# Kernel tuning notes

Measured on AMD Instinct MI355X. Metric: run time of the kernel, lower is better.

## Reference

```python
import jax, jax.numpy as jnp
import numpy as np

D_MODEL = 1024
N_HEADS = 16
HEAD_DIM = D_MODEL // N_HEADS
D_FF = 4096
MAX_STEPS = 16
MAX_LEN = 64  # hardcoded in the module
LN_EPS = 1e-5


def _layer_norm(x, g, b):
    m = jnp.mean(x, axis=-1, keepdims=True)
    v = jnp.mean((x - m) ** 2, axis=-1, keepdims=True)
    return (x - m) * jax.lax.rsqrt(v + LN_EPS) * g + b


def setup_inputs() -> dict:
    key = jax.random.key(0)
    ks = jax.random.split(key, 12)
    B, S = 8, 1024
    std = 0.02
    return {
        "x": jax.random.normal(ks[0], (B, S, D_MODEL), dtype=jnp.float32),
        "step_embed": jax.random.normal(ks[1], (MAX_STEPS, D_MODEL), dtype=jnp.float32) * std,
        "qkv_w": jax.random.normal(ks[2], (D_MODEL, 3 * D_MODEL), dtype=jnp.float32) * std,
        "qkv_b": jnp.zeros((3 * D_MODEL,), dtype=jnp.float32),
        "out_w": jax.random.normal(ks[3], (D_MODEL, D_MODEL), dtype=jnp.float32) * std,
        "out_b": jnp.zeros((D_MODEL,), dtype=jnp.float32),
        "rel_pos_bias": jax.random.normal(ks[4], (2 * MAX_LEN - 1,), dtype=jnp.float32) * std,
        "w1": jax.random.normal(ks[5], (D_MODEL, D_FF), dtype=jnp.float32) * std,
        "b1": jnp.zeros((D_FF,), dtype=jnp.float32),
        "w2": jax.random.normal(ks[6], (D_FF, D_MODEL), dtype=jnp.float32) * std,
        "b2": jnp.zeros((D_MODEL,), dtype=jnp.float32),
        "ln1_g": jnp.ones((D_MODEL,), dtype=jnp.float32),
        "ln1_b": jnp.zeros((D_MODEL,), dtype=jnp.float32),
        "ln2_g": jnp.ones((D_MODEL,), dtype=jnp.float32),
        "ln2_b": jnp.zeros((D_MODEL,), dtype=jnp.float32),
        "think_step": 3,
    }


def reference(x, step_embed, qkv_w, qkv_b, out_w, out_b, rel_pos_bias,
              w1, b1, w2, b2, ln1_g, ln1_b, ln2_g, ln2_b, think_step):
    B, S, D = x.shape
    scale = HEAD_DIM ** -0.5

    # step embedding (clamped), broadcast over batch and sequence
    step = min(int(think_step), MAX_STEPS - 1)
    x = x + step_embed[step][None, None, :]

    # QKV projection -> (3, B, H, S, Dh)
    qkv = (x @ qkv_w + qkv_b).reshape(B, S, 3, N_HEADS, HEAD_DIM)
    qkv = jnp.transpose(qkv, (2, 0, 3, 1, 4))
    q, k, v = qkv[0], qkv[1], qkv[2]

    # attention scores with clamped relative-position bias
    scores = jnp.einsum("bhqd,bhkd->bhqk", q, k) * scale
    pos = jnp.arange(S)
    rel = jnp.clip(pos[:, None] - pos[None, :] + (MAX_LEN - 1), 0, 2 * MAX_LEN - 2)
    scores = scores + rel_pos_bias[rel][None, None, :, :]

    probs = jax.nn.softmax(scores, axis=-1)
    attn = jnp.einsum("bhqk,bhkd->bhqd", probs, v)
    attn = jnp.transpose(attn, (0, 2, 1, 3)).reshape(B, S, D)
    attn = attn @ out_w + out_b

    x = _layer_norm(x + attn, ln1_g, ln1_b)
    ffn = jax.nn.gelu(x @ w1 + b1, approximate=False) @ w2 + b2
    x = _layer_norm(x + ffn, ln2_g, ln2_b)
    return x
```

## Files before the change

### kernel.cpp

```cpp
#include <hip/hip_runtime.h>
#include <cstdint>
#include <cmath>

typedef unsigned short u16;
typedef unsigned int u32;
typedef __bf16 bf16x8 __attribute__((ext_vector_type(8)));
typedef float f32x4 __attribute__((ext_vector_type(4)));
typedef float f32x16 __attribute__((ext_vector_type(16)));

#define DEV __device__ __forceinline__

DEV u16 f2bf(float f) {
    union { float f; unsigned u; } a; a.f = f;
    unsigned u = a.u;
    return (u16)((u + 0x7FFFu + ((u >> 16) & 1u)) >> 16);
}

DEV u32 pack2bf(float a, float b) {
    union { float f; u32 u; } ua, ub; ua.f = a; ub.f = b;
    return __builtin_amdgcn_perm(ub.u + 0x8000u, ua.u + 0x8000u, 0x07060302u);
}

DEV float fast_exp2(float x) {
    float r;
    asm("v_exp_f32 %0, %1" : "=v"(r) : "v"(x));
    return r;
}

DEV void async16(void* lds, const void* g) {
    __builtin_amdgcn_global_load_lds(
        (const __attribute__((address_space(1))) unsigned int*)g,
        (__attribute__((address_space(3))) unsigned int*)lds, 16, 0, 0);
}

#define LOG2E 1.44269504088896f

__global__ __launch_bounds__(256)
void prep_k(const float* __restrict__ s0, u16* __restrict__ d0,
            const float* __restrict__ s1, u16* __restrict__ d1,
            const float* __restrict__ s2, u16* __restrict__ d2,
            const float* __restrict__ s3, u16* __restrict__ d3,
            const float* __restrict__ x, const float* __restrict__ se,
            const int* __restrict__ ts, float* __restrict__ xo, u16* __restrict__ xb) {
    int b = blockIdx.x, tid = threadIdx.x;
    if (b < 12288) {
        __shared__ float tile[32][33];
        const float* src; u16* dst; int N, tidx;
        if (b < 3072)      { src = s0; dst = d0; N = 3072; tidx = b; }
        else if (b < 4096) { src = s1; dst = d1; N = 1024; tidx = b - 3072; }
        else if (b < 8192) { src = s2; dst = d2; N = 4096; tidx = b - 4096; }
        else               { src = s3; dst = d3; N = 1024; tidx = b - 8192; }
        int ntx = N >> 5;
        int n0 = (tidx % ntx) * 32, k0 = (tidx / ntx) * 32;
        int K = (b >= 8192) ? 4096 : 1024;
        int tx = tid & 31, ty = tid >> 5;
        #pragma unroll
        for (int i = ty; i < 32; i += 8) tile[i][tx] = src[(size_t)(k0 + i) * N + n0 + tx];
        __syncthreads();
        #pragma unroll
        for (int i = ty; i < 32; i += 8) dst[(size_t)(n0 + i) * K + k0 + tx] = f2bf(tile[tx][i]);
    } else {
        int st = ts[0]; st = st < 0 ? 0 : (st > 15 ? 15 : st);
        size_t i = (size_t)(b - 12288) * 256 + tid;
        float4 v = ((const float4*)x)[i];
        int c = (int)(i & 255);
        float4 e = ((const float4*)(se + (size_t)st * 1024))[c];
        v.x += e.x; v.y += e.y; v.z += e.z; v.w += e.w;
        ((float4*)xo)[i] = v;
        ushort4 u; u.x = f2bf(v.x); u.y = f2bf(v.y); u.z = f2bf(v.z); u.w = f2bf(v.w);
        ((ushort4*)xb)[i] = u;
    }
}

template<int EPI>
__global__ __launch_bounds__(256)
void gemm_bt(const u16* __restrict__ A, const u16* __restrict__ Bt,
             const float* __restrict__ bias, int Kdim,
             u16* __restrict__ ob0, u16* __restrict__ ob1, u16* __restrict__ ob2,
             const float* __restrict__ addf, float* __restrict__ outf) {
    __shared__ __align__(16) u16 lA[128 * 64];
    __shared__ __align__(16) u16 lB[128 * 64];
    const int tid = threadIdx.x, wave = tid >> 6, lane = tid & 63;
    const int m5 = lane & 31, h = lane >> 5;
    const int wm = wave >> 1, wn = wave & 1;
    const size_t m0 = (size_t)blockIdx.x * 128, n0 = (size_t)blockIdx.y * 128;
    const size_t kb = (size_t)Kdim * 2;

    f32x16 acc[2][2];
    #pragma unroll
    for (int i = 0; i < 2; i++)
        #pragma unroll
        for (int j = 0; j < 2; j++)
            #pragma unroll
            for (int e = 0; e < 16; e++) acc[i][j][e] = 0.f;

    const char* Ab = (const char*)A + m0 * kb;
    const char* Bb = (const char*)Bt + n0 * kb;

    auto stage = [&](const char* srcbase, u16* ldsb, int k0) {
        #pragma unroll
        for (int j = 0; j < 4; j++) {
            int loff = wave * 4096 + j * 1024 + lane * 16;
            int L = loff >> 4, r = L >> 3, c = L & 7, g = c ^ (r & 7);
            async16((char*)ldsb + loff, srcbase + (size_t)r * kb + (size_t)k0 * 2 + g * 16);
        }
    };

    stage(Ab, lA, 0); stage(Bb, lB, 0);
    const int r7 = m5 & 7;
    for (int k0 = 0; k0 < Kdim; k0 += 64) {
        __syncthreads();
        bf16x8 af[2][4], bfr[2][4];
        #pragma unroll
        for (int ti = 0; ti < 2; ti++) {
            int rowA = wm * 64 + ti * 32 + m5;
            int rowB = wn * 64 + ti * 32 + m5;
            #pragma unroll
            for (int kh = 0; kh < 4; kh++) {
                int cs = (kh * 2 + h) ^ r7;
                af[ti][kh]  = *(const bf16x8*)((const char*)lA + rowA * 128 + cs * 16);
                bfr[ti][kh] = *(const bf16x8*)((const char*)lB + rowB * 128 + cs * 16);
            }
        }
        __syncthreads();
        if (k0 + 64 < Kdim) { stage(Ab, lA, k0 + 64); stage(Bb, lB, k0 + 64); }
        #pragma unroll
        for (int kh = 0; kh < 4; kh++)
            #pragma unroll
            for (int ti = 0; ti < 2; ti++)
                #pragma unroll
                for (int tj = 0; tj < 2; tj++)
                    acc[ti][tj] = __builtin_amdgcn_mfma_f32_32x32x16_bf16(
                        af[ti][kh], bfr[tj][kh], acc[ti][tj], 0, 0, 0);
    }

    #pragma unroll
    for (int ti = 0; ti < 2; ti++) {
        #pragma unroll
        for (int tj = 0; tj < 2; tj++) {
            size_t col = n0 + wn * 64 + tj * 32 + m5;
            float bv = bias[col];
            if constexpr (EPI == 0) {
                size_t t = col >> 10, c = col & 1023, hh = c >> 6, dh = c & 63;
                #pragma unroll
                for (int g = 0; g < 4; g++) {
                    size_t row0 = m0 + wm * 64 + ti * 32 + 4 * h + 8 * g;
                    size_t bq = row0 >> 10, s0 = row0 & 1023;
                    if (t == 0) {
                        #pragma unroll
                        for (int r = 0; r < 4; r++)
                            ob0[((bq * 16 + hh) * 1024 + s0 + r) * 64 + dh] =
                                f2bf((acc[ti][tj][g * 4 + r] + bv) * 0.18033688011112f);
                    } else if (t == 1) {
                        #pragma unroll
                        for (int r = 0; r < 4; r++)
                            ob1[((bq * 16 + hh) * 1024 + s0 + r) * 64 + dh] =
                                f2bf(acc[ti][tj][g * 4 + r] + bv);
                    } else {
                        ushort4 tmp;
                        tmp.x = f2bf(acc[ti][tj][g * 4 + 0] + bv);
                        tmp.y = f2bf(acc[ti][tj][g * 4 + 1] + bv);
                        tmp.z = f2bf(acc[ti][tj][g * 4 + 2] + bv);
                        tmp.w = f2bf(acc[ti][tj][g * 4 + 3] + bv);
                        *(ushort4*)(ob2 + ((bq * 16 + hh) * 64 + dh) * 1024 + s0) = tmp;
                    }
                }
            } else {
                #pragma unroll
                for (int g = 0; g < 4; g++) {
                    #pragma unroll
                    for (int r = 0; r < 4; r++) {
                        size_t row = m0 + wm * 64 + ti * 32 + 4 * h + 8 * g + r;
                        float val = acc[ti][tj][g * 4 + r] + bv;
                        if constexpr (EPI == 1) {
                            size_t o = row * 1024 + col;
                            outf[o] = addf[o] + val;
                        } else if constexpr (EPI == 2) {
                            float ge = 0.5f * val * (1.f + erff(val * 0.70710678118f));
                            ob0[row * 4096 + col] = f2bf(ge);
                        } else {
                            size_t o = row * 1024 + col;
                            outf[o] = addf[o] + val;
                        }
                    }
                }
            }
        }
    }
}

__global__ __launch_bounds__(256, 2)
void attn_k(const u16* __restrict__ Q, const u16* __restrict__ K_, const u16* __restrict__ Vt,
            const float* __restrict__ relb, u16* __restrict__ Out) {
    __shared__ __align__(16) u16 sP[128 * 128];
    __shared__ __align__(16) u16 sK[128 * 64];
    __shared__ __align__(16) u16 sVt[64 * 128];
    __shared__ float sL[4][128];
    __shared__ float sLinv[128];
    __shared__ float sRel[128];

    const int tid = threadIdx.x, wave = tid >> 6, lane = tid & 63;
    const int m5 = lane & 31, h = lane >> 5;
    const int bh = blockIdx.x, q0 = blockIdx.y * 128;
    const size_t base = (size_t)bh * 65536;

    if (tid < 127) sRel[tid] = relb[tid] * LOG2E;

    auto stageK = [&](int kv0) {
        const char* kbp = (const char*)(K_ + base + (size_t)kv0 * 64);
        #pragma unroll
        for (int j = 0; j < 4; j++) {
            int loff = wave * 4096 + j * 1024 + lane * 16;
            int L = loff >> 4, r = L >> 3, c = L & 7, g = c ^ (r & 7);
            async16((char*)sK + loff, kbp + (size_t)r * 128 + g * 16);
        }
    };
    auto stageV = [&](int kv0) {
        const char* vbp = (const char*)(Vt + base) + (size_t)kv0 * 2;
        #pragma unroll
        for (int j = 0; j < 4; j++) {
            int loff = wave * 4096 + j * 1024 + lane * 16;
            int L = loff >> 4, r = L >> 4, c = L & 15, g = c ^ (r & 15);
            async16((char*)sVt + loff, vbp + (size_t)r * 2048 + g * 16);
        }
    };

    {
        const char* qb = (const char*)(Q + base + (size_t)q0 * 64);
        #pragma unroll
        for (int j = 0; j < 4; j++) {
            int loff = wave * 4096 + j * 1024 + lane * 16;
            int L = loff >> 4, r = L >> 3, c = L & 7, g = c ^ (r & 7);
            async16((char*)sP + loff, qb + (size_t)r * 128 + g * 16);
        }
    }
    stageK(0); stageV(0);
    __syncthreads();

    bf16x8 qf[4][4];
    #pragma unroll
    for (int qt = 0; qt < 4; qt++) {
        int row = qt * 32 + m5;
        #pragma unroll
        for (int s = 0; s < 4; s++) {
            int cs = (2 * s + h) ^ (m5 & 7);
            qf[qt][s] = *(const bf16x8*)((const char*)sP + row * 128 + cs * 16);
        }
    }
    __syncthreads();

    const int qh = wave >> 1, dhh = wave & 1;
    f32x16 Oacc[2];
    #pragma unroll
    for (int i = 0; i < 2; i++)
        #pragma unroll
        for (int e = 0; e < 16; e++) Oacc[i][e] = 0.f;
    float lsum[4] = {0.f, 0.f, 0.f, 0.f};

    for (int t = 0; t < 8; t++) {
        const int kv0 = t * 128;
        const int kvr = wave * 32 + m5;
        bf16x8 kf[4];
        #pragma unroll
        for (int s = 0; s < 4; s++) {
            int cs = (2 * s + h) ^ (m5 & 7);
            kf[s] = *(const bf16x8*)((const char*)sK + kvr * 128 + cs * 16);
        }
        f32x16 sc[4];
        #pragma unroll
        for (int qt = 0; qt < 4; qt++)
            #pragma unroll
            for (int e = 0; e < 16; e++) sc[qt][e] = 0.f;
        #pragma unroll
        for (int s = 0; s < 4; s++)
            #pragma unroll
            for (int qt = 0; qt < 4; qt++)
                sc[qt] = __builtin_amdgcn_mfma_f32_32x32x16_bf16(kf[s], qf[qt][s], sc[qt], 0, 0, 0);

        const int kvb = kv0 + wave * 32 + 4 * h;
        const bool far_lo = (kv0 >= q0 + 190);
        const bool far_hi = (kv0 <= q0 - 190);
        #pragma unroll
        for (int qt = 0; qt < 4; qt++) {
            const int qs = q0 + qt * 32 + m5;
            if (far_lo || far_hi) {
                float cb = far_lo ? sRel[0] : sRel[126];
                #pragma unroll
                for (int e = 0; e < 16; e++) sc[qt][e] = fast_exp2(sc[qt][e] + cb);
            } else {
                int relbase = qs - kvb + 63;
                #pragma unroll
                for (int g = 0; g < 4; g++)
                    #pragma unroll
                    for (int r = 0; r < 4; r++) {
                        int rel = relbase - 8 * g - r;
                        rel = rel < 0 ? 0 : (rel > 126 ? 126 : rel);
                        sc[qt][4 * g + r] = fast_exp2(sc[qt][4 * g + r] + sRel[rel]);
                    }
            }
            #pragma unroll
            for (int e = 0; e < 16; e++) lsum[qt] += sc[qt][e];
            u32 pk[4][2];
            #pragma unroll
            for (int g = 0; g < 4; g++) {
                pk[g][0] = pack2bf(sc[qt][4 * g + 0], sc[qt][4 * g + 1]);
                pk[g][1] = pack2bf(sc[qt][4 * g + 2], sc[qt][4 * g + 3]);
            }
            const int q = qt * 32 + m5;
            char* prow = (char*)sP + q * 256;
            #pragma unroll
            for (int u = 0; u < 2; u++) {
                u32 s0 = h ? pk[2 * u][0] : pk[2 * u + 1][0];
                u32 s1 = h ? pk[2 * u][1] : pk[2 * u + 1][1];
                u32 r0 = __shfl_xor((int)s0, 32);
                u32 r1 = __shfl_xor((int)s1, 32);
                uint4 w;
                if (h == 0) { w.x = pk[2 * u][0]; w.y = pk[2 * u][1]; w.z = r0; w.w = r1; }
                else        { w.x = r0; w.y = r1; w.z = pk[2 * u + 1][0]; w.w = pk[2 * u + 1][1]; }
                int c16 = (4 * wave + 2 * u + h) ^ (q & 15);
                *(uint4*)(prow + c16 * 16) = w;
            }
        }
        __syncthreads();
        if (t < 7) stageK(kv0 + 128);

        #pragma unroll
        for (int s = 0; s < 8; s++) {
            int dh = dhh * 32 + m5;
            int cv = (2 * s + h) ^ (dh & 15);
            bf16x8 vf = *(const bf16x8*)((const char*)sVt + dh * 256 + cv * 16);
            #pragma unroll
            for (int qt = 0; qt < 2; qt++) {
                int q = qh * 64 + qt * 32 + m5;
                int cp = (2 * s + h) ^ (q & 15);
                bf16x8 pf = *(const bf16x8*)((const char*)sP + q * 256 + cp * 16);
                Oacc[qt] = __builtin_amdgcn_mfma_f32_32x32x16_bf16(pf, vf, Oacc[qt], 0, 0, 0);
            }
        }
        __syncthreads();
        if (t < 7) stageV(kv0 + 128);
    }

    #pragma unroll
    for (int qt = 0; qt < 4; qt++) lsum[qt] += __shfl_xor(lsum[qt], 32);
    if (h == 0) {
        #pragma unroll
        for (int qt = 0; qt < 4; qt++) sL[wave][qt * 32 + m5] = lsum[qt];
    }
    __syncthreads();
    if (tid < 128) sLinv[tid] = 1.f / (sL[0][tid] + sL[1][tid] + sL[2][tid] + sL[3][tid]);
    __syncthreads();

    const int b = bh >> 4, hh = bh & 15;
    const int dh = dhh * 32 + m5;
    #pragma unroll
    for (int qt = 0; qt < 2; qt++) {
        #pragma unroll
        for (int g = 0; g < 4; g++) {
            #pragma unroll
            for (int r = 0; r < 4; r++) {
                int rl = qh * 64 + qt * 32 + 4 * h + 8 * g + r;
                float val = Oacc[qt][4 * g + r] * sLinv[rl];
                size_t s = (size_t)(q0 + rl);
                Out[((size_t)b * 1024 + s) * 1024 + hh * 64 + dh] = f2bf(val);
            }
        }
    }
}

template<bool WB>
__global__ __launch_bounds__(256)
void ln_k(const float* __restrict__ in, const float* __restrict__ g, const float* __restrict__ b,
          float* __restrict__ of, u16* __restrict__ ob) {
    __shared__ float ws1[4], ws2[4];
    int row = blockIdx.x, t = threadIdx.x;
    float4 v = ((const float4*)(in + (size_t)row * 1024))[t];
    float s = v.x + v.y + v.z + v.w;
    float s2 = v.x * v.x + v.y * v.y + v.z * v.z + v.w * v.w;
    #pragma unroll
    for (int m = 1; m < 64; m <<= 1) { s += __shfl_xor(s, m); s2 += __shfl_xor(s2, m); }
    if ((t & 63) == 0) { ws1[t >> 6] = s; ws2[t >> 6] = s2; }
    __syncthreads();
    s = ws1[0] + ws1[1] + ws1[2] + ws1[3];
    s2 = ws2[0] + ws2[1] + ws2[2] + ws2[3];
    float mean = s * (1.f / 1024.f);
    float var = s2 * (1.f / 1024.f) - mean * mean;
    float inv = rsqrtf(var + 1e-5f);
    float4 gv = ((const float4*)g)[t], bv = ((const float4*)b)[t];
    float4 o;
    o.x = (v.x - mean) * inv * gv.x + bv.x;
    o.y = (v.y - mean) * inv * gv.y + bv.y;
    o.z = (v.z - mean) * inv * gv.z + bv.z;
    o.w = (v.w - mean) * inv * gv.w + bv.w;
    ((float4*)(of + (size_t)row * 1024))[t] = o;
    if (WB) {
        ushort4 u; u.x = f2bf(o.x); u.y = f2bf(o.y); u.z = f2bf(o.z); u.w = f2bf(o.w);
        ((ushort4*)(ob + (size_t)row * 1024))[t] = u;
    }
}

extern "C" void kernel_launch(void* const* d_in, const int* in_sizes, int n_in,
                              void* d_out, int out_size, void* d_ws, size_t ws_size,
                              hipStream_t stream) {
    (void)in_sizes; (void)n_in; (void)out_size; (void)ws_size;
    const float* x          = (const float*)d_in[0];
    const float* step_embed = (const float*)d_in[1];
    const float* qkv_w      = (const float*)d_in[2];
    const float* qkv_b      = (const float*)d_in[3];
    const float* out_w      = (const float*)d_in[4];
    const float* out_b      = (const float*)d_in[5];
    const float* relb       = (const float*)d_in[6];
    const float* w1         = (const float*)d_in[7];
    const float* b1         = (const float*)d_in[8];
    const float* w2         = (const float*)d_in[9];
    const float* b2         = (const float*)d_in[10];
    const float* ln1g       = (const float*)d_in[11];
    const float* ln1b       = (const float*)d_in[12];
    const float* ln2g       = (const float*)d_in[13];
    const float* ln2b       = (const float*)d_in[14];
    const int*   tstep      = (const int*)d_in[15];
    float* out = (float*)d_out;

    char* p = (char*)d_ws;
    u16* wt_qkv = (u16*)p; p += (size_t)3072 * 1024 * 2;
    u16* wt_out = (u16*)p; p += (size_t)1024 * 1024 * 2;
    u16* wt_w1  = (u16*)p; p += (size_t)4096 * 1024 * 2;
    u16* wt_w2  = (u16*)p; p += (size_t)1024 * 4096 * 2;
    float* xse  = (float*)p; p += (size_t)8192 * 1024 * 4;
    u16* xseb   = (u16*)p; p += (size_t)8192 * 1024 * 2;
    u16* qbuf   = (u16*)p; p += (size_t)8192 * 1024 * 2;
    u16* kbuf   = (u16*)p; p += (size_t)8192 * 1024 * 2;
    u16* attnb  = (u16*)p; p += (size_t)8192 * 1024 * 2;
    float* res1 = (float*)p; p += (size_t)8192 * 1024 * 4;
    float* y1   = xse;
    u16*   y1b  = xseb;
    u16*   hbuf = qbuf;
    float* res2 = res1;
    u16*   vtb  = (u16*)res1;

    prep_k<<<dim3(12288 + 8192), dim3(256), 0, stream>>>(qkv_w, wt_qkv, out_w, wt_out,
                                                         w1, wt_w1, w2, wt_w2,
                                                         x, step_embed, tstep, xse, xseb);
    gemm_bt<0><<<dim3(64, 24), dim3(256), 0, stream>>>(xseb, wt_qkv, qkv_b, 1024,
                                                       qbuf, kbuf, vtb, (const float*)nullptr, (float*)nullptr);
    attn_k<<<dim3(128, 8), dim3(256), 0, stream>>>(qbuf, kbuf, vtb, relb, attnb);
    gemm_bt<1><<<dim3(64, 8), dim3(256), 0, stream>>>(attnb, wt_out, out_b, 1024,
                                                      (u16*)nullptr, (u16*)nullptr, (u16*)nullptr, xse, res1);
    ln_k<true><<<dim3(8192), dim3(256), 0, stream>>>(res1, ln1g, ln1b, y1, y1b);
    gemm_bt<2><<<dim3(64, 32), dim3(256), 0, stream>>>(y1b, wt_w1, b1, 1024,
                                                       hbuf, (u16*)nullptr, (u16*)nullptr, (const float*)nullptr, (float*)nullptr);
    gemm_bt<3><<<dim3(64, 8), dim3(256), 0, stream>>>(hbuf, wt_w2, b2, 4096,
                                                      (u16*)nullptr, (u16*)nullptr, (u16*)nullptr, y1, res2);
    ln_k<false><<<dim3(8192), dim3(256), 0, stream>>>(res2, ln2g, ln2b, out, (u16*)nullptr);
}
```

Before: 513.0 us.

## Add 256x256 pipelined 8-wave GEMM for QKV and FFN1 projections

Adds a new GEMM kernel with 256x256 output tiles, 512 threads and a double-buffered LDS layout that splits each 64-wide K tile into halves. The main loop interleaves async global-to-LDS staging with MFMA phases, using explicit waitcnt, barriers, sched_barrier and s_setprio to overlap loads with compute. The QKV and FFN-up projections switch to this kernel to raise data reuse per tile. The other GEMMs stay on the 128x128 kernel. The trade-off is 128KB of LDS per block, which allows only one block per CU, and a coarser grid that can leave a partial last wave (for example 384 blocks for QKV).

```diff
diff --git a/kernel.cpp b/kernel.cpp
--- a/kernel.cpp
+++ b/kernel.cpp
@@ -34,6 +34,14 @@
 }
 
 #define LOG2E 1.44269504088896f
+
+#define BAR()   __builtin_amdgcn_s_barrier()
+#define LGKM0() asm volatile("s_waitcnt lgkmcnt(0)" ::: "memory")
+#define VMW4()  asm volatile("s_waitcnt vmcnt(4)" ::: "memory")
+#define VMW0()  asm volatile("s_waitcnt vmcnt(0)" ::: "memory")
+#define SFEN()  __builtin_amdgcn_sched_barrier(0)
+#define PHI()   __builtin_amdgcn_s_setprio(1)
+#define PLO()   __builtin_amdgcn_s_setprio(0)
 
 __global__ __launch_bounds__(256)
 void prep_k(const float* __restrict__ s0, u16* __restrict__ d0,
@@ -73,69 +81,126 @@
 }
 
 template<int EPI>
-__global__ __launch_bounds__(256)
-void gemm_bt(const u16* __restrict__ A, const u16* __restrict__ Bt,
+__global__ __launch_bounds__(512, 2)
+void gemm256(const u16* __restrict__ A, const u16* __restrict__ Bt,
              const float* __restrict__ bias, int Kdim,
-             u16* __restrict__ ob0, u16* __restrict__ ob1, u16* __restrict__ ob2,
-             const float* __restrict__ addf, float* __restrict__ outf) {
-    __shared__ __align__(16) u16 lA[128 * 64];
-    __shared__ __align__(16) u16 lB[128 * 64];
+             u16* __restrict__ ob0, u16* __restrict__ ob1, u16* __restrict__ ob2) {
+    __shared__ __align__(16) char lds[131072];
     const int tid = threadIdx.x, wave = tid >> 6, lane = tid & 63;
     const int m5 = lane & 31, h = lane >> 5;
-    const int wm = wave >> 1, wn = wave & 1;
-    const size_t m0 = (size_t)blockIdx.x * 128, n0 = (size_t)blockIdx.y * 128;
+    const int wm = wave >> 2, wn = wave & 3;
+    const size_t m0 = (size_t)blockIdx.x * 256, n0 = (size_t)blockIdx.y * 256;
     const size_t kb = (size_t)Kdim * 2;
-
-    f32x16 acc[2][2];
-    #pragma unroll
-    for (int i = 0; i < 2; i++)
-        #pragma unroll
-        for (int j = 0; j < 2; j++)
-            #pragma unroll
-            for (int e = 0; e < 16; e++) acc[i][j][e] = 0.f;
-
+    const int NT = Kdim >> 6;
+
+    const int L0 = tid, L1 = 512 + tid;
+    const int r0 = L0 >> 2, r1 = L1 >> 2;
+    const size_t so0 = (size_t)r0 * kb + (size_t)(((L0 & 3) ^ ((r0 >> 1) & 3)) * 16);
+    const size_t so1 = (size_t)r1 * kb + (size_t)(((L1 & 3) ^ ((r1 >> 1) & 3)) * 16);
     const char* Ab = (const char*)A + m0 * kb;
     const char* Bb = (const char*)Bt + n0 * kb;
 
-    auto stage = [&](const char* srcbase, u16* ldsb, int k0) {
-        #pragma unroll
-        for (int j = 0; j < 4; j++) {
-            int loff = wave * 4096 + j * 1024 + lane * 16;
-            int L = loff >> 4, r = L >> 3, c = L & 7, g = c ^ (r & 7);
-            async16((char*)ldsb + loff, srcbase + (size_t)r * kb + (size_t)k0 * 2 + g * 16);
-        }
-    };
-
-    stage(Ab, lA, 0); stage(Bb, lB, 0);
-    const int r7 = m5 & 7;
-    for (int k0 = 0; k0 < Kdim; k0 += 64) {
-        __syncthreads();
-        bf16x8 af[2][4], bfr[2][4];
-        #pragma unroll
-        for (int ti = 0; ti < 2; ti++) {
-            int rowA = wm * 64 + ti * 32 + m5;
-            int rowB = wn * 64 + ti * 32 + m5;
-            #pragma unroll
-            for (int kh = 0; kh < 4; kh++) {
-                int cs = (kh * 2 + h) ^ r7;
-                af[ti][kh]  = *(const bf16x8*)((const char*)lA + rowA * 128 + cs * 16);
-                bfr[ti][kh] = *(const bf16x8*)((const char*)lB + rowB * 128 + cs * 16);
-            }
-        }
-        __syncthreads();
-        if (k0 + 64 < Kdim) { stage(Ab, lA, k0 + 64); stage(Bb, lB, k0 + 64); }
-        #pragma unroll
-        for (int kh = 0; kh < 4; kh++)
-            #pragma unroll
-            for (int ti = 0; ti < 2; ti++)
-                #pragma unroll
-                for (int tj = 0; tj < 2; tj++)
-                    acc[ti][tj] = __builtin_amdgcn_mfma_f32_32x32x16_bf16(
-                        af[ti][kh], bfr[tj][kh], acc[ti][tj], 0, 0, 0);
-    }
-
-    #pragma unroll
-    for (int ti = 0; ti < 2; ti++) {
+    f32x16 acc[4][2];
+    #pragma unroll
+    for (int i = 0; i < 4; i++)
+        #pragma unroll
+        for (int j = 0; j < 2; j++)
+            #pragma unroll
+            for (int e = 0; e < 16; e++) acc[i][j][e] = 0.f;
+
+    bf16x8 af[4][2], bfr[2];
+
+    auto stage = [&](int matB, int db, int kh2, int tile) {
+        char* dst = (char*)lds + matB * 65536 + db * 32768 + kh2 * 16384;
+        const char* src = (matB ? Bb : Ab) + (size_t)(tile * 128 + kh2 * 64);
+        async16(dst + L0 * 16, src + so0);
+        async16(dst + L1 * 16, src + so1);
+    };
+    auto readA = [&](int db, int kh2) {
+        const char* base = (const char*)lds + db * 32768 + kh2 * 16384;
+        #pragma unroll
+        for (int ti = 0; ti < 4; ti++) {
+            int r = wm * 128 + ti * 32 + m5;
+            const char* rb = base + r * 64;
+            int sx = (r >> 1) & 3;
+            af[ti][0] = *(const bf16x8*)(rb + ((h ^ sx) << 4));
+            af[ti][1] = *(const bf16x8*)(rb + (((2 + h) ^ sx) << 4));
+        }
+    };
+    auto readB = [&](int db, int kh2, int tj) {
+        const char* base = (const char*)lds + 65536 + db * 32768 + kh2 * 16384;
+        int r = wn * 64 + tj * 32 + m5;
+        const char* rb = base + r * 64;
+        int sx = (r >> 1) & 3;
+        bfr[0] = *(const bf16x8*)(rb + ((h ^ sx) << 4));
+        bfr[1] = *(const bf16x8*)(rb + (((2 + h) ^ sx) << 4));
+    };
+    auto mma = [&](int tj) {
+        #pragma unroll
+        for (int kk = 0; kk < 2; kk++)
+            #pragma unroll
+            for (int ti = 0; ti < 4; ti++)
+                acc[ti][tj] = __builtin_amdgcn_mfma_f32_32x32x16_bf16(
+                    af[ti][kk], bfr[kk], acc[ti][tj], 0, 0, 0);
+    };
+
+    stage(0, 0, 0, 0); stage(1, 0, 0, 0);
+    stage(0, 0, 1, 0); stage(1, 0, 1, 0);
+    stage(0, 1, 0, 1); stage(1, 1, 0, 1);
+    VMW4(); BAR(); SFEN();
+
+    const int NIT = NT >> 1;
+    for (int it = 0; it < NIT; ++it) {
+        const int t = 2 * it;
+        const bool s2 = (t + 2 < NT);
+        readA(0, 0); readB(0, 0, 0);
+        stage(0, 1, 1, t + 1);
+        BAR(); LGKM0(); SFEN();
+        PHI(); mma(0); PLO();
+        BAR();
+        readB(0, 0, 1);
+        stage(1, 1, 1, t + 1);
+        BAR(); LGKM0(); SFEN();
+        PHI(); mma(1); PLO();
+        BAR();
+        readA(0, 1); readB(0, 1, 0);
+        if (s2) stage(0, 0, 0, t + 2);
+        BAR(); LGKM0(); SFEN();
+        PHI(); mma(0); PLO();
+        BAR();
+        readB(0, 1, 1);
+        if (s2) stage(1, 0, 0, t + 2);
+        BAR(); LGKM0(); SFEN();
+        PHI(); mma(1); PLO();
+        if (s2) { VMW4(); } else { VMW0(); }
+        BAR(); SFEN();
+        readA(1, 0); readB(1, 0, 0);
+        if (s2) stage(0, 0, 1, t + 2);
+        BAR(); LGKM0(); SFEN();
+        PHI(); mma(0); PLO();
+        BAR();
+        readB(1, 0, 1);
+        if (s2) stage(1, 0, 1, t + 2);
+        BAR(); LGKM0(); SFEN();
+        PHI(); mma(1); PLO();
+        BAR();
+        readA(1, 1); readB(1, 1, 0);
+        if (s2) stage(0, 1, 0, t + 3);
+        BAR(); LGKM0(); SFEN();
+        PHI(); mma(0); PLO();
+        BAR();
+        readB(1, 1, 1);
+        if (s2) stage(1, 1, 0, t + 3);
+        BAR(); LGKM0(); SFEN();
+        PHI(); mma(1); PLO();
+        if (it + 1 < NIT) {
+            VMW4();
+            BAR(); SFEN();
+        }
+    }
+
+    #pragma unroll
+    for (int ti = 0; ti < 4; ti++) {
         #pragma unroll
         for (int tj = 0; tj < 2; tj++) {
             size_t col = n0 + wn * 64 + tj * 32 + m5;
@@ -144,7 +209,7 @@
                 size_t t = col >> 10, c = col & 1023, hh = c >> 6, dh = c & 63;
                 #pragma unroll
                 for (int g = 0; g < 4; g++) {
-                    size_t row0 = m0 + wm * 64 + ti * 32 + 4 * h + 8 * g;
+                    size_t row0 = m0 + wm * 128 + ti * 32 + 4 * h + 8 * g;
                     size_t bq = row0 >> 10, s0 = row0 & 1023;
                     if (t == 0) {
                         #pragma unroll
@@ -167,21 +232,99 @@
                 }
             } else {
                 #pragma unroll
-                for (int g = 0; g < 4; g++) {
+                for (int g = 0; g < 4; g++)
                     #pragma unroll
                     for (int r = 0; r < 4; r++) {
-                        size_t row = m0 + wm * 64 + ti * 32 + 4 * h + 8 * g + r;
+                        size_t row = m0 + wm * 128 + ti * 32 + 4 * h + 8 * g + r;
                         float val = acc[ti][tj][g * 4 + r] + bv;
-                        if constexpr (EPI == 1) {
-                            size_t o = row * 1024 + col;
-                            outf[o] = addf[o] + val;
-                        } else if constexpr (EPI == 2) {
-                            float ge = 0.5f * val * (1.f + erff(val * 0.70710678118f));
-                            ob0[row * 4096 + col] = f2bf(ge);
-                        } else {
-                            size_t o = row * 1024 + col;
-                            outf[o] = addf[o] + val;
-                        }
+                        float ge = 0.5f * val * (1.f + erff(val * 0.70710678118f));
+                        ob0[row * 4096 + col] = f2bf(ge);
+                    }
+            }
+        }
+    }
+}
+
+template<int EPI>
+__global__ __launch_bounds__(256)
+void gemm_bt(const u16* __restrict__ A, const u16* __restrict__ Bt,
+             const float* __restrict__ bias, int Kdim,
+             u16* __restrict__ ob0, u16* __restrict__ ob1, u16* __restrict__ ob2,
+             const float* __restrict__ addf, float* __restrict__ outf) {
+    __shared__ __align__(16) u16 lA[128 * 64];
+    __shared__ __align__(16) u16 lB[128 * 64];
+    const int tid = threadIdx.x, wave = tid >> 6, lane = tid & 63;
+    const int m5 = lane & 31, h = lane >> 5;
+    const int wm = wave >> 1, wn = wave & 1;
+    const size_t m0 = (size_t)blockIdx.x * 128, n0 = (size_t)blockIdx.y * 128;
+    const size_t kb = (size_t)Kdim * 2;
+
+    f32x16 acc[2][2];
+    #pragma unroll
+    for (int i = 0; i < 2; i++)
+        #pragma unroll
+        for (int j = 0; j < 2; j++)
+            #pragma unroll
+            for (int e = 0; e < 16; e++) acc[i][j][e] = 0.f;
+
+    const char* Ab = (const char*)A + m0 * kb;
+    const char* Bb = (const char*)Bt + n0 * kb;
+
+    auto stage = [&](const char* srcbase, u16* ldsb, int k0) {
+        #pragma unroll
+        for (int j = 0; j < 4; j++) {
+            int loff = wave * 4096 + j * 1024 + lane * 16;
+            int L = loff >> 4, r = L >> 3, c = L & 7, g = c ^ (r & 7);
+            async16((char*)ldsb + loff, srcbase + (size_t)r * kb + (size_t)k0 * 2 + g * 16);
+        }
+    };
+
+    stage(Ab, lA, 0); stage(Bb, lB, 0);
+    const int r7 = m5 & 7;
+    for (int k0 = 0; k0 < Kdim; k0 += 64) {
+        __syncthreads();
+        bf16x8 af[2][4], bfr[2][4];
+        #pragma unroll
+        for (int ti = 0; ti < 2; ti++) {
+            int rowA = wm * 64 + ti * 32 + m5;
+            int rowB = wn * 64 + ti * 32 + m5;
+            #pragma unroll
+            for (int kh = 0; kh < 4; kh++) {
+                int cs = (kh * 2 + h) ^ r7;
+                af[ti][kh]  = *(const bf16x8*)((const char*)lA + rowA * 128 + cs * 16);
+                bfr[ti][kh] = *(const bf16x8*)((const char*)lB + rowB * 128 + cs * 16);
+            }
+        }
+        __syncthreads();
+        if (k0 + 64 < Kdim) { stage(Ab, lA, k0 + 64); stage(Bb, lB, k0 + 64); }
+        #pragma unroll
+        for (int kh = 0; kh < 4; kh++)
+            #pragma unroll
+            for (int ti = 0; ti < 2; ti++)
+                #pragma unroll
+                for (int tj = 0; tj < 2; tj++)
+                    acc[ti][tj] = __builtin_amdgcn_mfma_f32_32x32x16_bf16(
+                        af[ti][kh], bfr[tj][kh], acc[ti][tj], 0, 0, 0);
+    }
+
+    #pragma unroll
+    for (int ti = 0; ti < 2; ti++) {
+        #pragma unroll
+        for (int tj = 0; tj < 2; tj++) {
+            size_t col = n0 + wn * 64 + tj * 32 + m5;
+            float bv = bias[col];
+            #pragma unroll
+            for (int g = 0; g < 4; g++) {
+                #pragma unroll
+                for (int r = 0; r < 4; r++) {
+                    size_t row = m0 + wm * 64 + ti * 32 + 4 * h + 8 * g + r;
+                    float val = acc[ti][tj][g * 4 + r] + bv;
+                    if constexpr (EPI == 1 || EPI == 3) {
+                        size_t o = row * 1024 + col;
+                        outf[o] = addf[o] + val;
+                    } else if constexpr (EPI == 2) {
+                        float ge = 0.5f * val * (1.f + erff(val * 0.70710678118f));
+                        ob0[row * 4096 + col] = f2bf(ge);
                     }
                 }
             }
@@ -441,14 +584,14 @@
     prep_k<<<dim3(12288 + 8192), dim3(256), 0, stream>>>(qkv_w, wt_qkv, out_w, wt_out,
                                                          w1, wt_w1, w2, wt_w2,
                                                          x, step_embed, tstep, xse, xseb);
-    gemm_bt<0><<<dim3(64, 24), dim3(256), 0, stream>>>(xseb, wt_qkv, qkv_b, 1024,
-                                                       qbuf, kbuf, vtb, (const float*)nullptr, (float*)nullptr);
+    gemm256<0><<<dim3(32, 12), dim3(512), 0, stream>>>(xseb, wt_qkv, qkv_b, 1024,
+                                                       qbuf, kbuf, vtb);
     attn_k<<<dim3(128, 8), dim3(256), 0, stream>>>(qbuf, kbuf, vtb, relb, attnb);
     gemm_bt<1><<<dim3(64, 8), dim3(256), 0, stream>>>(attnb, wt_out, out_b, 1024,
                                                       (u16*)nullptr, (u16*)nullptr, (u16*)nullptr, xse, res1);
     ln_k<true><<<dim3(8192), dim3(256), 0, stream>>>(res1, ln1g, ln1b, y1, y1b);
-    gemm_bt<2><<<dim3(64, 32), dim3(256), 0, stream>>>(y1b, wt_w1, b1, 1024,
-                                                       hbuf, (u16*)nullptr, (u16*)nullptr, (const float*)nullptr, (float*)nullptr);
+    gemm256<2><<<dim3(32, 16), dim3(512), 0, stream>>>(y1b, wt_w1, b1, 1024,
+                                                       hbuf, (u16*)nullptr, (u16*)nullptr);
     gemm_bt<3><<<dim3(64, 8), dim3(256), 0, stream>>>(hbuf, wt_w2, b2, 4096,
                                                       (u16*)nullptr, (u16*)nullptr, (u16*)nullptr, y1, res2);
     ln_k<false><<<dim3(8192), dim3(256), 0, stream>>>(res2, ln2g, ln2b, out, (u16*)nullptr);
```

New measurement: 643.7 us. +25.5%, slower.
